# Performance work log

Measured on AMD Instinct MI355X. Metric: run time of the kernel, lower is better.

The kernel has to match this reference:

```python
import jax, jax.numpy as jnp
import numpy as np

N_QUBITS = 5
N_LAYERS = 3
DIM = 2 ** N_QUBITS  # 32


def _apply_ry(state, theta, w):
    # state: [B, 32] complex64; theta: scalar or [B] float32
    half = theta * 0.5
    c = jnp.cos(half)
    s = jnp.sin(half)
    if c.ndim:  # per-sample angles
        c = c[:, None, None]
        s = s[:, None, None]
    pre, post = 2 ** w, 2 ** (N_QUBITS - 1 - w)
    st = state.reshape(-1, pre, 2, post)
    s0, s1 = st[:, :, 0, :], st[:, :, 1, :]
    out = jnp.stack([c * s0 - s * s1, s * s0 + c * s1], axis=2)
    return out.reshape(-1, DIM)


def _apply_rz(state, theta, w):
    half = theta * 0.5
    e0 = jnp.exp(-1j * half)
    e1 = jnp.exp(1j * half)
    pre, post = 2 ** w, 2 ** (N_QUBITS - 1 - w)
    st = state.reshape(-1, pre, 2, post)
    out = jnp.stack([e0 * st[:, :, 0, :], e1 * st[:, :, 1, :]], axis=2)
    return out.reshape(-1, DIM)


def _apply_cnot(state, c):
    # control wire c, target wire c+1 (adjacent, as in the CNOT chain)
    pre, post = 2 ** c, 2 ** (N_QUBITS - 2 - c)
    st = state.reshape(-1, pre, 2, 2, post)
    out = jnp.stack([st[:, :, 0], st[:, :, 1, ::-1, :]], axis=2)
    return out.reshape(-1, DIM)


def _expval_z(state, w):
    pre, post = 2 ** w, 2 ** (N_QUBITS - 1 - w)
    p = jnp.abs(state.reshape(-1, pre, 2, post)) ** 2
    return (p[:, :, 0, :] - p[:, :, 1, :]).sum(axis=(1, 2))


def _circuit(enc, qp):
    # enc: [B, 5] in [-1,1]; qp: [30]
    B = enc.shape[0]
    state = jnp.zeros((B, DIM), jnp.complex64).at[:, 0].set(1.0)
    pi = jnp.float32(np.pi)
    for i in range(N_QUBITS):
        state = _apply_ry(state, enc[:, i] * pi, i)
    idx = 0
    for _ in range(N_LAYERS):
        for i in range(N_QUBITS):
            state = _apply_ry(state, qp[idx], i); idx += 1
            state = _apply_rz(state, qp[idx], i); idx += 1
        for i in range(N_QUBITS - 1):
            state = _apply_cnot(state, i)
    return jnp.stack([_expval_z(state, i) for i in range(N_QUBITS)], axis=1)


def setup_inputs() -> dict:
    key = jax.random.key(0)
    ks = jax.random.split(key, 14)
    B, S, A = 131072, 252, 4
    def lin(k, fin, fout):
        return jax.random.normal(k, (fin, fout), jnp.float32) / jnp.sqrt(jnp.float32(fin))
    return {
        'state': jax.random.normal(ks[0], (B, S), jnp.float32),
        'W1': lin(ks[1], S, 128), 'b1': jnp.zeros((128,), jnp.float32),
        'W2': lin(ks[2], 128, 64), 'b2': jnp.zeros((64,), jnp.float32),
        'W3': lin(ks[3], 64, N_QUBITS), 'b3': jnp.zeros((N_QUBITS,), jnp.float32),
        'qp': jax.random.normal(ks[4], (N_LAYERS * N_QUBITS * 2,), jnp.float32) * 0.1,
        'D1': lin(ks[5], N_QUBITS, 32), 'd1': jnp.zeros((32,), jnp.float32),
        'D2': lin(ks[6], 32, 16), 'd2': jnp.zeros((16,), jnp.float32),
        'D3': lin(ks[7], 16, A), 'd3': jnp.zeros((A,), jnp.float32),
    }


def reference(state, W1, b1, W2, b2, W3, b3, qp, D1, d1, D2, d2, D3, d3):
    h = jax.nn.relu(state @ W1 + b1)
    h = jax.nn.relu(h @ W2 + b2)
    enc = jnp.tanh(h @ W3 + b3)          # [B, 5]
    q = _circuit(enc, qp)                # [B, 5] PauliZ expectations
    h = jax.nn.relu(q @ D1 + d1)
    h = jax.nn.relu(h @ D2 + d2)
    return h @ D3 + d3                   # [B, action_dim]
```

## Files before the change

### kernel.cpp

```cpp
#include <hip/hip_runtime.h>
#include <hip/hip_bf16.h>
#include <math.h>

typedef _Float16 half8_t __attribute__((ext_vector_type(8)));
typedef _Float16 half4_t __attribute__((ext_vector_type(4)));
typedef float floatx4 __attribute__((ext_vector_type(4)));

__device__ __forceinline__ void prep_body(const float* __restrict__ W,
                                          _Float16* __restrict__ dst,
                                          int K, int N, int KS, int b) {
    int ks   = b % KS;
    int nt   = b / KS;
    int lane = threadIdx.x;
    int col  = nt * 16 + (lane & 15);
    int kbase = ks * 32 + ((lane >> 4) << 3);
    half8_t v;
#pragma unroll
    for (int j = 0; j < 8; ++j) {
        int k = kbase + j;
        float x = (k < K && col < N) ? W[(size_t)k * N + col] : 0.f;
        v[j] = (_Float16)x;
    }
    *(half8_t*)(dst + (size_t)(b * 64 + lane) * 8) = v;
}

__global__ void prep_all(const float* __restrict__ W1, const float* __restrict__ W2,
                         const float* __restrict__ W3,
                         _Float16* __restrict__ w1f, _Float16* __restrict__ w2f,
                         _Float16* __restrict__ w3f) {
    int b = blockIdx.x;
    if (b < 64)      prep_body(W1, w1f, 252, 128, 8, b);
    else if (b < 80) prep_body(W2, w2f, 128, 64, 4, b - 64);
    else             prep_body(W3, w3f, 64, 5, 2, b - 80);
}

__global__ __launch_bounds__(256, 3) void front_kernel(
    const float* __restrict__ state,
    const _Float16* __restrict__ w1f, const float* __restrict__ b1,
    const _Float16* __restrict__ w2f, const float* __restrict__ b2,
    const _Float16* __restrict__ w3f, const float* __restrict__ b3,
    float* __restrict__ enc) {
    __shared__ char lds[32768];
    const int tid = threadIdx.x;
    const int w   = tid >> 6;
    const int l   = tid & 63;
    const int l15 = l & 15;
    const int lhi = l >> 4;
    const int wrow = w * 16;
    const int rowbase = blockIdx.x * 64;

    {
        const int srow = wrow + (l >> 2);
        const int sc   = (l & 3) * 4;
        const float* Arow = state + (size_t)(rowbase + srow) * 252;
        const int swz = (srow & 7) << 4;
#pragma unroll
        for (int i = 0; i < 16; ++i) {
            int cf = i * 16 + sc;
            half4_t h;
            if (cf < 252) {
                floatx4 f = *(const floatx4*)(Arow + cf);
                h = half4_t{ (_Float16)f[0], (_Float16)f[1], (_Float16)f[2], (_Float16)f[3] };
            } else {
                h = half4_t{ 0, 0, 0, 0 };
            }
            int cb = cf * 2;
            *(half4_t*)(lds + (srow << 9) + (cb ^ swz)) = h;
        }
    }

    half8_t bw1[2][8], bw2[4], bw3[2];
#pragma unroll
    for (int ntl = 0; ntl < 2; ++ntl)
#pragma unroll
        for (int ks = 0; ks < 8; ++ks)
            bw1[ntl][ks] = *(const half8_t*)(w1f + (size_t)(((w * 2 + ntl) * 8 + ks) * 64 + l) * 8);
#pragma unroll
    for (int ks = 0; ks < 4; ++ks)
        bw2[ks] = *(const half8_t*)(w2f + (size_t)((w * 4 + ks) * 64 + l) * 8);
#pragma unroll
    for (int ks = 0; ks < 2; ++ks)
        bw3[ks] = *(const half8_t*)(w3f + (size_t)(ks * 64 + l) * 8);

    __syncthreads();

    floatx4 acc1[4][2];
#pragma unroll
    for (int mi = 0; mi < 4; ++mi)
#pragma unroll
        for (int ntl = 0; ntl < 2; ++ntl) acc1[mi][ntl] = floatx4{0, 0, 0, 0};

#pragma unroll
    for (int ks = 0; ks < 8; ++ks) {
        half8_t a[4];
#pragma unroll
        for (int mi = 0; mi < 4; ++mi) {
            int r = mi * 16 + l15;
            int cb = ks * 64 + lhi * 16;
            a[mi] = *(const half8_t*)(lds + (r << 9) + (cb ^ ((r & 7) << 4)));
        }
#pragma unroll
        for (int mi = 0; mi < 4; ++mi) {
#pragma unroll
            for (int ntl = 0; ntl < 2; ++ntl)
                acc1[mi][ntl] = __builtin_amdgcn_mfma_f32_16x16x32_f16(a[mi], bw1[ntl][ks], acc1[mi][ntl], 0, 0, 0);
        }
    }
    __syncthreads();

#pragma unroll
    for (int ntl = 0; ntl < 2; ++ntl) {
        int col = (w * 2 + ntl) * 16 + l15;
        float bb = b1[col];
#pragma unroll
        for (int mi = 0; mi < 4; ++mi) {
#pragma unroll
            for (int ri = 0; ri < 4; ++ri) {
                int row = mi * 16 + lhi * 4 + ri;
                float v = acc1[mi][ntl][ri] + bb;
                v = v > 0.f ? v : 0.f;
                *(_Float16*)(lds + (row << 8) + ((col * 2) ^ ((row & 7) << 4))) = (_Float16)v;
            }
        }
    }
    __syncthreads();

    floatx4 acc2[4];
#pragma unroll
    for (int mi = 0; mi < 4; ++mi) acc2[mi] = floatx4{0, 0, 0, 0};
#pragma unroll
    for (int ks = 0; ks < 4; ++ks) {
#pragma unroll
        for (int mi = 0; mi < 4; ++mi) {
            int r = mi * 16 + l15;
            int cb = ks * 64 + lhi * 16;
            half8_t a = *(const half8_t*)(lds + (r << 8) + (cb ^ ((r & 7) << 4)));
            acc2[mi] = __builtin_amdgcn_mfma_f32_16x16x32_f16(a, bw2[ks], acc2[mi], 0, 0, 0);
        }
    }

    {
        int col = w * 16 + l15;
        float bb = b2[col];
#pragma unroll
        for (int mi = 0; mi < 4; ++mi) {
#pragma unroll
            for (int ri = 0; ri < 4; ++ri) {
                int row = mi * 16 + lhi * 4 + ri;
                float v = acc2[mi][ri] + bb;
                v = v > 0.f ? v : 0.f;
                *(_Float16*)(lds + 16384 + (row << 7) + ((col * 2) ^ ((row & 7) << 4))) = (_Float16)v;
            }
        }
    }
    __syncthreads();

    floatx4 acc3 = floatx4{0, 0, 0, 0};
#pragma unroll
    for (int ks = 0; ks < 2; ++ks) {
        int r = wrow + l15;
        int cb = ks * 64 + lhi * 16;
        half8_t a = *(const half8_t*)(lds + 16384 + (r << 7) + (cb ^ ((r & 7) << 4)));
        acc3 = __builtin_amdgcn_mfma_f32_16x16x32_f16(a, bw3[ks], acc3, 0, 0, 0);
    }

    if (l15 < 5) {
        float bb = b3[l15];
#pragma unroll
        for (int ri = 0; ri < 4; ++ri) {
            int row = rowbase + wrow + lhi * 4 + ri;
            enc[(size_t)row * 5 + l15] = tanhf(acc3[ri] + bb);
        }
    }
}

template<int P>
__device__ __forceinline__ void ry_g(float* re, float* im, float c, float s) {
    constexpr int STR = 1 << P;
#pragma unroll
    for (int base = 0; base < 32; base += 2 * STR)
#pragma unroll
        for (int d = 0; d < STR; ++d) {
            int i0 = base + d, i1 = i0 + STR;
            float r0 = re[i0], r1 = re[i1], m0 = im[i0], m1 = im[i1];
            re[i0] = c * r0 - s * r1;  re[i1] = s * r0 + c * r1;
            im[i0] = c * m0 - s * m1;  im[i1] = s * m0 + c * m1;
        }
}

template<int P>
__device__ __forceinline__ void rz_g(float* re, float* im, float c, float s) {
#pragma unroll
    for (int i = 0; i < 32; ++i) {
        float t = ((i >> P) & 1) ? s : -s;
        float r = re[i], m = im[i];
        re[i] = c * r - t * m;
        im[i] = c * m + t * r;
    }
}

template<int PC, int PT>
__device__ __forceinline__ void cnot_g(float* re, float* im) {
#pragma unroll
    for (int i = 0; i < 32; ++i) {
        if (((i >> PC) & 1) && !((i >> PT) & 1)) {
            int j = i | (1 << PT);
            float t;
            t = re[i]; re[i] = re[j]; re[j] = t;
            t = im[i]; im[i] = im[j]; im[j] = t;
        }
    }
}

__global__ __launch_bounds__(256) void back_kernel(
    const float* __restrict__ enc, const float* __restrict__ qp,
    const float* __restrict__ D1, const float* __restrict__ d1,
    const float* __restrict__ D2, const float* __restrict__ d2,
    const float* __restrict__ D3, const float* __restrict__ d3,
    float* __restrict__ out) {
    __shared__ float sD1[160], sd1[32], sD2[512], sd2[16], sD3[64], sd3[4];
    __shared__ float sQc[30], sQs[30];
    const int tid = threadIdx.x;
    for (int i = tid; i < 512; i += 256) sD2[i] = D2[i];
    if (tid < 160) sD1[tid] = D1[tid];
    if (tid < 32)  sd1[tid] = d1[tid];
    if (tid < 64)  sD3[tid] = D3[tid];
    if (tid < 16)  sd2[tid] = d2[tid];
    if (tid < 4)   sd3[tid] = d3[tid];
    if (tid < 30) { float h = 0.5f * qp[tid]; sQc[tid] = cosf(h); sQs[tid] = sinf(h); }
    __syncthreads();

    const size_t r = (size_t)blockIdx.x * 256 + tid;

    float cq[5], sq[5];
    const float HPI = 1.57079632679489662f;
#pragma unroll
    for (int i = 0; i < 5; ++i) {
        float a = enc[r * 5 + i] * HPI;
        cq[i] = cosf(a);
        sq[i] = sinf(a);
    }
    float re[32], im[32];
#pragma unroll
    for (int i = 0; i < 32; ++i) {
        float v = ((i >> 4) & 1) ? sq[0] : cq[0];
        v *= ((i >> 3) & 1) ? sq[1] : cq[1];
        v *= ((i >> 2) & 1) ? sq[2] : cq[2];
        v *= ((i >> 1) & 1) ? sq[3] : cq[3];
        v *= ( i       & 1) ? sq[4] : cq[4];
        re[i] = v;
        im[i] = 0.f;
    }

#pragma unroll
    for (int lay = 0; lay < 3; ++lay) {
        const float* c = sQc + lay * 10;
        const float* s = sQs + lay * 10;
        ry_g<4>(re, im, c[0], s[0]);  rz_g<4>(re, im, c[1], s[1]);
        ry_g<3>(re, im, c[2], s[2]);  rz_g<3>(re, im, c[3], s[3]);
        ry_g<2>(re, im, c[4], s[4]);  rz_g<2>(re, im, c[5], s[5]);
        ry_g<1>(re, im, c[6], s[6]);  rz_g<1>(re, im, c[7], s[7]);
        ry_g<0>(re, im, c[8], s[8]);  rz_g<0>(re, im, c[9], s[9]);
        cnot_g<4, 3>(re, im);
        cnot_g<3, 2>(re, im);
        cnot_g<2, 1>(re, im);
        cnot_g<1, 0>(re, im);
    }

    float q[5] = {0, 0, 0, 0, 0};
#pragma unroll
    for (int i = 0; i < 32; ++i) {
        float p = re[i] * re[i] + im[i] * im[i];
        q[0] += ((i >> 4) & 1) ? -p : p;
        q[1] += ((i >> 3) & 1) ? -p : p;
        q[2] += ((i >> 2) & 1) ? -p : p;
        q[3] += ((i >> 1) & 1) ? -p : p;
        q[4] += ( i       & 1) ? -p : p;
    }

    float h1[32];
#pragma unroll
    for (int j = 0; j < 32; ++j) {
        float a = sd1[j];
#pragma unroll
        for (int k = 0; k < 5; ++k) a += q[k] * sD1[k * 32 + j];
        h1[j] = a > 0.f ? a : 0.f;
    }
    float h2[16];
#pragma unroll
    for (int j = 0; j < 16; ++j) {
        float a = sd2[j];
#pragma unroll
        for (int k = 0; k < 32; ++k) a += h1[k] * sD2[k * 16 + j];
        h2[j] = a > 0.f ? a : 0.f;
    }
    floatx4 o;
#pragma unroll
    for (int j = 0; j < 4; ++j) {
        float a = sd3[j];
#pragma unroll
        for (int k = 0; k < 16; ++k) a += h2[k] * sD3[k * 4 + j];
        o[j] = a;
    }
    *(floatx4*)(out + r * 4) = o;
}

extern "C" void kernel_launch(void* const* d_in, const int* in_sizes, int n_in,
                              void* d_out, int out_size, void* d_ws, size_t ws_size,
                              hipStream_t stream) {
    const float* state = (const float*)d_in[0];
    const float* W1 = (const float*)d_in[1];
    const float* b1 = (const float*)d_in[2];
    const float* W2 = (const float*)d_in[3];
    const float* b2 = (const float*)d_in[4];
    const float* W3 = (const float*)d_in[5];
    const float* b3 = (const float*)d_in[6];
    const float* qp = (const float*)d_in[7];
    const float* D1 = (const float*)d_in[8];
    const float* d1 = (const float*)d_in[9];
    const float* D2 = (const float*)d_in[10];
    const float* d2 = (const float*)d_in[11];
    const float* D3 = (const float*)d_in[12];
    const float* d3 = (const float*)d_in[13];
    float* out = (float*)d_out;

    const int B = in_sizes[0] / 252;

    char* ws = (char*)d_ws;
    _Float16* w1f = (_Float16*)ws;
    _Float16* w2f = (_Float16*)(ws + 65536);
    _Float16* w3f = (_Float16*)(ws + 65536 + 16384);
    float*    enc = (float*)(ws + 65536 + 16384 + 2048);

    prep_all<<<82, 64, 0, stream>>>(W1, W2, W3, w1f, w2f, w3f);
    front_kernel<<<B / 64, 256, 0, stream>>>(state, w1f, b1, w2f, b2, w3f, b3, enc);
    back_kernel<<<B / 256, 256, 0, stream>>>(enc, qp, D1, d1, D2, d2, D3, d3, out);
}
```

Measured before the change: 61.68 us.

## Make front kernel persistent over four row tiles with register prefetch

Each block of the front MLP kernel now processes four 64-row tiles in sequence. The weight fragments are loaded into registers once per block instead of once per tile. The global loads for the next tile's input rows go into registers while the current tile's three MFMA layers run, and the LDS is split into separate regions so staging and the hidden-layer buffers do not conflict. The aim is to hide HBM latency and amortize the weight loads, at the cost of more registers and LDS, a launch bound lowered from 3 to 2 blocks per CU, and a quarter as many blocks.

```diff
diff --git a/kernel.cpp b/kernel.cpp
--- a/kernel.cpp
+++ b/kernel.cpp
@@ -5,6 +5,8 @@
 typedef _Float16 half8_t __attribute__((ext_vector_type(8)));
 typedef _Float16 half4_t __attribute__((ext_vector_type(4)));
 typedef float floatx4 __attribute__((ext_vector_type(4)));
+
+#define TILES 4
 
 __device__ __forceinline__ void prep_body(const float* __restrict__ W,
                                           _Float16* __restrict__ dst,
@@ -34,144 +36,155 @@
     else             prep_body(W3, w3f, 64, 5, 2, b - 80);
 }
 
-__global__ __launch_bounds__(256, 3) void front_kernel(
+__global__ __launch_bounds__(256, 2) void front_kernel(
     const float* __restrict__ state,
     const _Float16* __restrict__ w1f, const float* __restrict__ b1,
     const _Float16* __restrict__ w2f, const float* __restrict__ b2,
     const _Float16* __restrict__ w3f, const float* __restrict__ b3,
     float* __restrict__ enc) {
-    __shared__ char lds[32768];
+    __shared__ char lds[57344];
     const int tid = threadIdx.x;
     const int w   = tid >> 6;
     const int l   = tid & 63;
     const int l15 = l & 15;
     const int lhi = l >> 4;
     const int wrow = w * 16;
-    const int rowbase = blockIdx.x * 64;
-
-    {
-        const int srow = wrow + (l >> 2);
-        const int sc   = (l & 3) * 4;
-        const float* Arow = state + (size_t)(rowbase + srow) * 252;
-        const int swz = (srow & 7) << 4;
+    const int row0 = blockIdx.x * (64 * TILES);
+
+    const int srow = wrow + (l >> 2);
+    const int sc   = (l & 3) * 4;
+    const int swz  = (srow & 7) << 4;
+
+    half8_t bw1[2][8], bw2[4], bw3[2];
+#pragma unroll
+    for (int ntl = 0; ntl < 2; ++ntl)
+#pragma unroll
+        for (int ks = 0; ks < 8; ++ks)
+            bw1[ntl][ks] = *(const half8_t*)(w1f + (size_t)(((w * 2 + ntl) * 8 + ks) * 64 + l) * 8);
+#pragma unroll
+    for (int ks = 0; ks < 4; ++ks)
+        bw2[ks] = *(const half8_t*)(w2f + (size_t)((w * 4 + ks) * 64 + l) * 8);
+#pragma unroll
+    for (int ks = 0; ks < 2; ++ks)
+        bw3[ks] = *(const half8_t*)(w3f + (size_t)(ks * 64 + l) * 8);
+
+    floatx4 pf[16];
+
+#define ISSUE_A(TILE)                                                           \
+    {                                                                           \
+        const float* Arow = state + (size_t)(row0 + (TILE) * 64 + srow) * 252;  \
+        _Pragma("unroll")                                                       \
+        for (int i = 0; i < 16; ++i) {                                          \
+            int cf = i * 16 + sc;                                               \
+            if (cf < 252) pf[i] = *(const floatx4*)(Arow + cf);                 \
+        }                                                                       \
+    }
+
+    ISSUE_A(0)
+
+#pragma unroll
+    for (int t = 0; t < TILES; ++t) {
 #pragma unroll
         for (int i = 0; i < 16; ++i) {
             int cf = i * 16 + sc;
             half4_t h;
             if (cf < 252) {
-                floatx4 f = *(const floatx4*)(Arow + cf);
+                floatx4 f = pf[i];
                 h = half4_t{ (_Float16)f[0], (_Float16)f[1], (_Float16)f[2], (_Float16)f[3] };
             } else {
                 h = half4_t{ 0, 0, 0, 0 };
             }
-            int cb = cf * 2;
-            *(half4_t*)(lds + (srow << 9) + (cb ^ swz)) = h;
-        }
-    }
-
-    half8_t bw1[2][8], bw2[4], bw3[2];
-#pragma unroll
-    for (int ntl = 0; ntl < 2; ++ntl)
-#pragma unroll
-        for (int ks = 0; ks < 8; ++ks)
-            bw1[ntl][ks] = *(const half8_t*)(w1f + (size_t)(((w * 2 + ntl) * 8 + ks) * 64 + l) * 8);
-#pragma unroll
-    for (int ks = 0; ks < 4; ++ks)
-        bw2[ks] = *(const half8_t*)(w2f + (size_t)((w * 4 + ks) * 64 + l) * 8);
-#pragma unroll
-    for (int ks = 0; ks < 2; ++ks)
-        bw3[ks] = *(const half8_t*)(w3f + (size_t)(ks * 64 + l) * 8);
-
-    __syncthreads();
-
-    floatx4 acc1[4][2];
-#pragma unroll
-    for (int mi = 0; mi < 4; ++mi)
-#pragma unroll
-        for (int ntl = 0; ntl < 2; ++ntl) acc1[mi][ntl] = floatx4{0, 0, 0, 0};
-
-#pragma unroll
-    for (int ks = 0; ks < 8; ++ks) {
-        half8_t a[4];
-#pragma unroll
-        for (int mi = 0; mi < 4; ++mi) {
-            int r = mi * 16 + l15;
+            *(half4_t*)(lds + (srow << 9) + ((cf * 2) ^ swz)) = h;
+        }
+        __syncthreads();
+
+        if (t + 1 < TILES) ISSUE_A(t + 1)
+
+        floatx4 acc1[4][2];
+#pragma unroll
+        for (int mi = 0; mi < 4; ++mi)
+#pragma unroll
+            for (int ntl = 0; ntl < 2; ++ntl) acc1[mi][ntl] = floatx4{0, 0, 0, 0};
+
+#pragma unroll
+        for (int ks = 0; ks < 8; ++ks) {
+            half8_t a[4];
+#pragma unroll
+            for (int mi = 0; mi < 4; ++mi) {
+                int r = mi * 16 + l15;
+                int cb = ks * 64 + lhi * 16;
+                a[mi] = *(const half8_t*)(lds + (r << 9) + (cb ^ ((r & 7) << 4)));
+            }
+#pragma unroll
+            for (int mi = 0; mi < 4; ++mi)
+#pragma unroll
+                for (int ntl = 0; ntl < 2; ++ntl)
+                    acc1[mi][ntl] = __builtin_amdgcn_mfma_f32_16x16x32_f16(a[mi], bw1[ntl][ks], acc1[mi][ntl], 0, 0, 0);
+        }
+
+#pragma unroll
+        for (int ntl = 0; ntl < 2; ++ntl) {
+            int col = (w * 2 + ntl) * 16 + l15;
+            float bb = b1[col];
+#pragma unroll
+            for (int mi = 0; mi < 4; ++mi)
+#pragma unroll
+                for (int ri = 0; ri < 4; ++ri) {
+                    int row = mi * 16 + lhi * 4 + ri;
+                    float v = acc1[mi][ntl][ri] + bb;
+                    v = v > 0.f ? v : 0.f;
+                    *(_Float16*)(lds + 32768 + (row << 8) + ((col * 2) ^ ((row & 7) << 4))) = (_Float16)v;
+                }
+        }
+        __syncthreads();
+
+        floatx4 acc2[4];
+#pragma unroll
+        for (int mi = 0; mi < 4; ++mi) acc2[mi] = floatx4{0, 0, 0, 0};
+#pragma unroll
+        for (int ks = 0; ks < 4; ++ks)
+#pragma unroll
+            for (int mi = 0; mi < 4; ++mi) {
+                int r = mi * 16 + l15;
+                int cb = ks * 64 + lhi * 16;
+                half8_t a = *(const half8_t*)(lds + 32768 + (r << 8) + (cb ^ ((r & 7) << 4)));
+                acc2[mi] = __builtin_amdgcn_mfma_f32_16x16x32_f16(a, bw2[ks], acc2[mi], 0, 0, 0);
+            }
+
+        {
+            int col = w * 16 + l15;
+            float bb = b2[col];
+#pragma unroll
+            for (int mi = 0; mi < 4; ++mi)
+#pragma unroll
+                for (int ri = 0; ri < 4; ++ri) {
+                    int row = mi * 16 + lhi * 4 + ri;
+                    float v = acc2[mi][ri] + bb;
+                    v = v > 0.f ? v : 0.f;
+                    *(_Float16*)(lds + 49152 + (row << 7) + ((col * 2) ^ ((row & 7) << 4))) = (_Float16)v;
+                }
+        }
+        __syncthreads();
+
+        floatx4 acc3 = floatx4{0, 0, 0, 0};
+#pragma unroll
+        for (int ks = 0; ks < 2; ++ks) {
+            int r = wrow + l15;
             int cb = ks * 64 + lhi * 16;
-            a[mi] = *(const half8_t*)(lds + (r << 9) + (cb ^ ((r & 7) << 4)));
-        }
-#pragma unroll
-        for (int mi = 0; mi < 4; ++mi) {
-#pragma unroll
-            for (int ntl = 0; ntl < 2; ++ntl)
-                acc1[mi][ntl] = __builtin_amdgcn_mfma_f32_16x16x32_f16(a[mi], bw1[ntl][ks], acc1[mi][ntl], 0, 0, 0);
-        }
-    }
-    __syncthreads();
-
-#pragma unroll
-    for (int ntl = 0; ntl < 2; ++ntl) {
-        int col = (w * 2 + ntl) * 16 + l15;
-        float bb = b1[col];
-#pragma unroll
-        for (int mi = 0; mi < 4; ++mi) {
+            half8_t a = *(const half8_t*)(lds + 49152 + (r << 7) + (cb ^ ((r & 7) << 4)));
+            acc3 = __builtin_amdgcn_mfma_f32_16x16x32_f16(a, bw3[ks], acc3, 0, 0, 0);
+        }
+
+        if (l15 < 5) {
+            float bb = b3[l15];
 #pragma unroll
             for (int ri = 0; ri < 4; ++ri) {
-                int row = mi * 16 + lhi * 4 + ri;
-                float v = acc1[mi][ntl][ri] + bb;
-                v = v > 0.f ? v : 0.f;
-                *(_Float16*)(lds + (row << 8) + ((col * 2) ^ ((row & 7) << 4))) = (_Float16)v;
+                int row = row0 + t * 64 + wrow + lhi * 4 + ri;
+                enc[(size_t)row * 5 + l15] = tanhf(acc3[ri] + bb);
             }
         }
     }
-    __syncthreads();
-
-    floatx4 acc2[4];
-#pragma unroll
-    for (int mi = 0; mi < 4; ++mi) acc2[mi] = floatx4{0, 0, 0, 0};
-#pragma unroll
-    for (int ks = 0; ks < 4; ++ks) {
-#pragma unroll
-        for (int mi = 0; mi < 4; ++mi) {
-            int r = mi * 16 + l15;
-            int cb = ks * 64 + lhi * 16;
-            half8_t a = *(const half8_t*)(lds + (r << 8) + (cb ^ ((r & 7) << 4)));
-            acc2[mi] = __builtin_amdgcn_mfma_f32_16x16x32_f16(a, bw2[ks], acc2[mi], 0, 0, 0);
-        }
-    }
-
-    {
-        int col = w * 16 + l15;
-        float bb = b2[col];
-#pragma unroll
-        for (int mi = 0; mi < 4; ++mi) {
-#pragma unroll
-            for (int ri = 0; ri < 4; ++ri) {
-                int row = mi * 16 + lhi * 4 + ri;
-                float v = acc2[mi][ri] + bb;
-                v = v > 0.f ? v : 0.f;
-                *(_Float16*)(lds + 16384 + (row << 7) + ((col * 2) ^ ((row & 7) << 4))) = (_Float16)v;
-            }
-        }
-    }
-    __syncthreads();
-
-    floatx4 acc3 = floatx4{0, 0, 0, 0};
-#pragma unroll
-    for (int ks = 0; ks < 2; ++ks) {
-        int r = wrow + l15;
-        int cb = ks * 64 + lhi * 16;
-        half8_t a = *(const half8_t*)(lds + 16384 + (r << 7) + (cb ^ ((r & 7) << 4)));
-        acc3 = __builtin_amdgcn_mfma_f32_16x16x32_f16(a, bw3[ks], acc3, 0, 0, 0);
-    }
-
-    if (l15 < 5) {
-        float bb = b3[l15];
-#pragma unroll
-        for (int ri = 0; ri < 4; ++ri) {
-            int row = rowbase + wrow + lhi * 4 + ri;
-            enc[(size_t)row * 5 + l15] = tanhf(acc3[ri] + bb);
-        }
-    }
+#undef ISSUE_A
 }
 
 template<int P>
@@ -333,6 +346,6 @@
     float*    enc = (float*)(ws + 65536 + 16384 + 2048);
 
     prep_all<<<82, 64, 0, stream>>>(W1, W2, W3, w1f, w2f, w3f);
-    front_kernel<<<B / 64, 256, 0, stream>>>(state, w1f, b1, w2f, b2, w3f, b3, enc);
+    front_kernel<<<B / (64 * TILES), 256, 0, stream>>>(state, w1f, b1, w2f, b2, w3f, b3, enc);
     back_kernel<<<B / 256, 256, 0, stream>>>(enc, qp, D1, d1, D2, d2, D3, d3, out);
 }
```

Result: slower. 86.87 us (+40.8%).

## Make front kernel persistent over row tiles with register prefetch of next tile

Applied to the files above, without the earlier changes.

The front MLP kernel now processes 8 tiles of 32 rows per block in a loop. The global loads for the next tile are issued into registers while the current tile's MFMA work runs, and the weight fragments are loaded once per block. Barriers become raw s_barrier calls with a wait on LDS counters only. The enc buffer changes to a column-major layout so the back kernel's loads coalesce, and tanh, sin and cos switch to fast approximate intrinsics. This trades occupancy (launch bounds drop from 3 to 2) and some accuracy for overlap of memory loads with compute.

```diff
diff --git a/kernel.cpp b/kernel.cpp
--- a/kernel.cpp
+++ b/kernel.cpp
@@ -5,6 +5,19 @@
 typedef _Float16 half8_t __attribute__((ext_vector_type(8)));
 typedef _Float16 half4_t __attribute__((ext_vector_type(4)));
 typedef float floatx4 __attribute__((ext_vector_type(4)));
+
+#define TPT 8
+
+__device__ __forceinline__ void lds_barrier() {
+    asm volatile("s_waitcnt lgkmcnt(0)" ::: "memory");
+    __builtin_amdgcn_s_barrier();
+    asm volatile("" ::: "memory");
+}
+
+__device__ __forceinline__ float fast_tanh(float x) {
+    float e = __expf(2.f * x);
+    return 1.f - 2.f / (e + 1.f);
+}
 
 __device__ __forceinline__ void prep_body(const float* __restrict__ W,
                                           _Float16* __restrict__ dst,
@@ -34,40 +47,37 @@
     else             prep_body(W3, w3f, 64, 5, 2, b - 80);
 }
 
-__global__ __launch_bounds__(256, 3) void front_kernel(
+__global__ __launch_bounds__(256, 2) void front_kernel(
     const float* __restrict__ state,
     const _Float16* __restrict__ w1f, const float* __restrict__ b1,
     const _Float16* __restrict__ w2f, const float* __restrict__ b2,
     const _Float16* __restrict__ w3f, const float* __restrict__ b3,
-    float* __restrict__ enc) {
-    __shared__ char lds[32768];
+    float* __restrict__ enc, int Btot) {
+    __shared__ char lds[28672];
     const int tid = threadIdx.x;
     const int w   = tid >> 6;
     const int l   = tid & 63;
     const int l15 = l & 15;
     const int lhi = l >> 4;
-    const int wrow = w * 16;
-    const int rowbase = blockIdx.x * 64;
-
-    {
-        const int srow = wrow + (l >> 2);
-        const int sc   = (l & 3) * 4;
-        const float* Arow = state + (size_t)(rowbase + srow) * 252;
-        const int swz = (srow & 7) << 4;
-#pragma unroll
-        for (int i = 0; i < 16; ++i) {
-            int cf = i * 16 + sc;
-            half4_t h;
-            if (cf < 252) {
-                floatx4 f = *(const floatx4*)(Arow + cf);
-                h = half4_t{ (_Float16)f[0], (_Float16)f[1], (_Float16)f[2], (_Float16)f[3] };
-            } else {
-                h = half4_t{ 0, 0, 0, 0 };
-            }
-            int cb = cf * 2;
-            *(half4_t*)(lds + (srow << 9) + (cb ^ swz)) = h;
-        }
-    }
+    const int row0 = blockIdx.x * (32 * TPT);
+
+    const int srow = tid >> 3;
+    const int sc0  = tid & 7;
+    const int sswz = (srow & 7) << 4;
+
+    floatx4 pf[8];
+
+#define ISSUE_A(T)                                                          \
+    {                                                                       \
+        const float* Ar = state + (size_t)(row0 + (T) * 32 + srow) * 252;   \
+        _Pragma("unroll")                                                   \
+        for (int jj = 0; jj < 8; ++jj) {                                    \
+            int c = sc0 + jj * 8;                                           \
+            if (c < 63) pf[jj] = *(const floatx4*)(Ar + c * 4);             \
+        }                                                                   \
+    }
+
+    ISSUE_A(0)
 
     half8_t bw1[2][8], bw2[4], bw3[2];
 #pragma unroll
@@ -82,96 +92,108 @@
     for (int ks = 0; ks < 2; ++ks)
         bw3[ks] = *(const half8_t*)(w3f + (size_t)(ks * 64 + l) * 8);
 
-    __syncthreads();
-
-    floatx4 acc1[4][2];
-#pragma unroll
-    for (int mi = 0; mi < 4; ++mi)
-#pragma unroll
-        for (int ntl = 0; ntl < 2; ++ntl) acc1[mi][ntl] = floatx4{0, 0, 0, 0};
-
-#pragma unroll
-    for (int ks = 0; ks < 8; ++ks) {
-        half8_t a[4];
-#pragma unroll
-        for (int mi = 0; mi < 4; ++mi) {
-            int r = mi * 16 + l15;
-            int cb = ks * 64 + lhi * 16;
-            a[mi] = *(const half8_t*)(lds + (r << 9) + (cb ^ ((r & 7) << 4)));
-        }
-#pragma unroll
-        for (int mi = 0; mi < 4; ++mi) {
-#pragma unroll
-            for (int ntl = 0; ntl < 2; ++ntl)
-                acc1[mi][ntl] = __builtin_amdgcn_mfma_f32_16x16x32_f16(a[mi], bw1[ntl][ks], acc1[mi][ntl], 0, 0, 0);
-        }
-    }
-    __syncthreads();
-
-#pragma unroll
-    for (int ntl = 0; ntl < 2; ++ntl) {
-        int col = (w * 2 + ntl) * 16 + l15;
-        float bb = b1[col];
-#pragma unroll
-        for (int mi = 0; mi < 4; ++mi) {
-#pragma unroll
-            for (int ri = 0; ri < 4; ++ri) {
-                int row = mi * 16 + lhi * 4 + ri;
-                float v = acc1[mi][ntl][ri] + bb;
-                v = v > 0.f ? v : 0.f;
-                *(_Float16*)(lds + (row << 8) + ((col * 2) ^ ((row & 7) << 4))) = (_Float16)v;
-            }
-        }
-    }
-    __syncthreads();
-
-    floatx4 acc2[4];
-#pragma unroll
-    for (int mi = 0; mi < 4; ++mi) acc2[mi] = floatx4{0, 0, 0, 0};
-#pragma unroll
-    for (int ks = 0; ks < 4; ++ks) {
-#pragma unroll
-        for (int mi = 0; mi < 4; ++mi) {
-            int r = mi * 16 + l15;
-            int cb = ks * 64 + lhi * 16;
-            half8_t a = *(const half8_t*)(lds + (r << 8) + (cb ^ ((r & 7) << 4)));
-            acc2[mi] = __builtin_amdgcn_mfma_f32_16x16x32_f16(a, bw2[ks], acc2[mi], 0, 0, 0);
-        }
-    }
-
-    {
-        int col = w * 16 + l15;
-        float bb = b2[col];
-#pragma unroll
-        for (int mi = 0; mi < 4; ++mi) {
-#pragma unroll
-            for (int ri = 0; ri < 4; ++ri) {
-                int row = mi * 16 + lhi * 4 + ri;
-                float v = acc2[mi][ri] + bb;
-                v = v > 0.f ? v : 0.f;
-                *(_Float16*)(lds + 16384 + (row << 7) + ((col * 2) ^ ((row & 7) << 4))) = (_Float16)v;
-            }
-        }
-    }
-    __syncthreads();
-
-    floatx4 acc3 = floatx4{0, 0, 0, 0};
-#pragma unroll
-    for (int ks = 0; ks < 2; ++ks) {
-        int r = wrow + l15;
-        int cb = ks * 64 + lhi * 16;
-        half8_t a = *(const half8_t*)(lds + 16384 + (r << 7) + (cb ^ ((r & 7) << 4)));
-        acc3 = __builtin_amdgcn_mfma_f32_16x16x32_f16(a, bw3[ks], acc3, 0, 0, 0);
-    }
-
-    if (l15 < 5) {
-        float bb = b3[l15];
-#pragma unroll
-        for (int ri = 0; ri < 4; ++ri) {
-            int row = rowbase + wrow + lhi * 4 + ri;
-            enc[(size_t)row * 5 + l15] = tanhf(acc3[ri] + bb);
-        }
-    }
+#pragma unroll 1
+    for (int t = 0; t < TPT; ++t) {
+#pragma unroll
+        for (int jj = 0; jj < 8; ++jj) {
+            int c = sc0 + jj * 8;
+            half4_t h;
+            if (c == 63) {
+                h = half4_t{0, 0, 0, 0};
+            } else {
+                floatx4 f = pf[jj];
+                h = half4_t{ (_Float16)f[0], (_Float16)f[1], (_Float16)f[2], (_Float16)f[3] };
+            }
+            *(half4_t*)(lds + (srow << 9) + ((c * 8) ^ sswz)) = h;
+        }
+        if (t + 1 < TPT) ISSUE_A(t + 1)
+        lds_barrier();
+
+        floatx4 acc1[2][2];
+#pragma unroll
+        for (int mi = 0; mi < 2; ++mi)
+#pragma unroll
+            for (int ntl = 0; ntl < 2; ++ntl) acc1[mi][ntl] = floatx4{0, 0, 0, 0};
+#pragma unroll
+        for (int ks = 0; ks < 8; ++ks) {
+            half8_t a[2];
+#pragma unroll
+            for (int mi = 0; mi < 2; ++mi) {
+                int r = mi * 16 + l15;
+                int cb = ks * 64 + lhi * 16;
+                a[mi] = *(const half8_t*)(lds + (r << 9) + (cb ^ ((r & 7) << 4)));
+            }
+#pragma unroll
+            for (int mi = 0; mi < 2; ++mi)
+#pragma unroll
+                for (int ntl = 0; ntl < 2; ++ntl)
+                    acc1[mi][ntl] = __builtin_amdgcn_mfma_f32_16x16x32_f16(a[mi], bw1[ntl][ks], acc1[mi][ntl], 0, 0, 0);
+        }
+
+#pragma unroll
+        for (int ntl = 0; ntl < 2; ++ntl) {
+            int col = (w * 2 + ntl) * 16 + l15;
+            float bb = b1[col];
+#pragma unroll
+            for (int mi = 0; mi < 2; ++mi)
+#pragma unroll
+                for (int ri = 0; ri < 4; ++ri) {
+                    int row = mi * 16 + lhi * 4 + ri;
+                    float v = acc1[mi][ntl][ri] + bb;
+                    v = v > 0.f ? v : 0.f;
+                    *(_Float16*)(lds + 16384 + (row << 8) + ((col * 2) ^ ((row & 7) << 4))) = (_Float16)v;
+                }
+        }
+        lds_barrier();
+
+        floatx4 acc2[2];
+#pragma unroll
+        for (int mi = 0; mi < 2; ++mi) acc2[mi] = floatx4{0, 0, 0, 0};
+#pragma unroll
+        for (int ks = 0; ks < 4; ++ks)
+#pragma unroll
+            for (int mi = 0; mi < 2; ++mi) {
+                int r = mi * 16 + l15;
+                int cb = ks * 64 + lhi * 16;
+                half8_t a = *(const half8_t*)(lds + 16384 + (r << 8) + (cb ^ ((r & 7) << 4)));
+                acc2[mi] = __builtin_amdgcn_mfma_f32_16x16x32_f16(a, bw2[ks], acc2[mi], 0, 0, 0);
+            }
+
+        {
+            int col = w * 16 + l15;
+            float bb = b2[col];
+#pragma unroll
+            for (int mi = 0; mi < 2; ++mi)
+#pragma unroll
+                for (int ri = 0; ri < 4; ++ri) {
+                    int row = mi * 16 + lhi * 4 + ri;
+                    float v = acc2[mi][ri] + bb;
+                    v = v > 0.f ? v : 0.f;
+                    *(_Float16*)(lds + 24576 + (row << 7) + ((col * 2) ^ ((row & 7) << 4))) = (_Float16)v;
+                }
+        }
+        lds_barrier();
+
+        if (w < 2) {
+            floatx4 acc3 = floatx4{0, 0, 0, 0};
+#pragma unroll
+            for (int ks = 0; ks < 2; ++ks) {
+                int r = w * 16 + l15;
+                int cb = ks * 64 + lhi * 16;
+                half8_t a = *(const half8_t*)(lds + 24576 + (r << 7) + (cb ^ ((r & 7) << 4)));
+                acc3 = __builtin_amdgcn_mfma_f32_16x16x32_f16(a, bw3[ks], acc3, 0, 0, 0);
+            }
+            if (l15 < 5) {
+                float bb = b3[l15];
+#pragma unroll
+                for (int ri = 0; ri < 4; ++ri) {
+                    int grow = row0 + t * 32 + w * 16 + lhi * 4 + ri;
+                    enc[(size_t)l15 * Btot + grow] = fast_tanh(acc3[ri] + bb);
+                }
+            }
+        }
+    }
+#undef ISSUE_A
 }
 
 template<int P>
@@ -217,7 +239,7 @@
     const float* __restrict__ D1, const float* __restrict__ d1,
     const float* __restrict__ D2, const float* __restrict__ d2,
     const float* __restrict__ D3, const float* __restrict__ d3,
-    float* __restrict__ out) {
+    float* __restrict__ out, int Btot) {
     __shared__ float sD1[160], sd1[32], sD2[512], sd2[16], sD3[64], sd3[4];
     __shared__ float sQc[30], sQs[30];
     const int tid = threadIdx.x;
@@ -236,9 +258,9 @@
     const float HPI = 1.57079632679489662f;
 #pragma unroll
     for (int i = 0; i < 5; ++i) {
-        float a = enc[r * 5 + i] * HPI;
-        cq[i] = cosf(a);
-        sq[i] = sinf(a);
+        float a = enc[(size_t)i * Btot + r] * HPI;
+        cq[i] = __cosf(a);
+        sq[i] = __sinf(a);
     }
     float re[32], im[32];
 #pragma unroll
@@ -333,6 +355,6 @@
     float*    enc = (float*)(ws + 65536 + 16384 + 2048);
 
     prep_all<<<82, 64, 0, stream>>>(W1, W2, W3, w1f, w2f, w3f);
-    front_kernel<<<B / 64, 256, 0, stream>>>(state, w1f, b1, w2f, b2, w3f, b3, enc);
-    back_kernel<<<B / 256, 256, 0, stream>>>(enc, qp, D1, d1, D2, d2, D3, d3, out);
-}
+    front_kernel<<<B / (32 * TPT), 256, 0, stream>>>(state, w1f, b1, w2f, b2, w3f, b3, enc, B);
+    back_kernel<<<B / 256, 256, 0, stream>>>(enc, qp, D1, d1, D2, d2, D3, d3, out, B);
+}
```

Result: faster. 56.46 us (-8.5%).
